# Kernel optimization log

Measured on AMD Instinct MI355X. Metric: run time of the kernel, lower is better.

The kernel has to match this reference:

```python
import jax, jax.numpy as jnp
import numpy as np

N = 50000      # nodes
E = 800000     # edges
D_IN = 128
D_H = 256
D_OUT = 128
EPS = 1e-5
SLOPE = 0.01   # LeakyReLU negative_slope


def setup_inputs() -> dict:
    key = jax.random.key(0)
    ks = jax.random.split(key, 24)
    inp = {}
    inp["x"] = jax.random.normal(ks[0], (N, D_IN), dtype=jnp.float32)
    inp["edge_index"] = jax.random.randint(ks[1], (2, E), 0, N, dtype=jnp.int32)
    dims = [(D_IN, D_H), (D_H, D_H), (D_H, D_H), (D_H, D_OUT)]
    for i, (di, do) in enumerate(dims, start=1):
        inp[f"W{i}"] = jax.random.normal(ks[4 * i - 2], (di, do), dtype=jnp.float32) / np.float32(np.sqrt(di))
        inp[f"b{i}"] = jnp.zeros((do,), dtype=jnp.float32)
        inp[f"g{i}"] = 1.0 + 0.1 * jax.random.normal(ks[4 * i - 1], (do,), dtype=jnp.float32)   # BN gamma
        inp[f"be{i}"] = 0.1 * jax.random.normal(ks[4 * i], (do,), dtype=jnp.float32)            # BN beta
    inp["ln_g"] = 1.0 + 0.1 * jax.random.normal(ks[18], (D_OUT,), dtype=jnp.float32)
    inp["ln_b"] = 0.1 * jax.random.normal(ks[19], (D_OUT,), dtype=jnp.float32)
    return inp


def _gcn_conv(x, W, b, src, dst, nisq):
    # PyG GCNConv: linear first, then sym-normalized aggregation with self-loops.
    xl = x @ W                                   # [N, do]
    coef = (nisq[src] * nisq[dst])[:, None]      # [E, 1]
    msg = xl[src] * coef                         # [E, do] gather
    agg = jax.ops.segment_sum(msg, dst, num_segments=N)  # scatter-add
    # self-loop contribution: deg^{-1/2}_i * deg^{-1/2}_i * xl_i
    return agg + xl * (nisq * nisq)[:, None] + b


def _bn(x, g, b):
    # BatchNorm1d, training-mode batch statistics (biased variance)
    m = jnp.mean(x, axis=0)
    v = jnp.var(x, axis=0)
    return (x - m) * jax.lax.rsqrt(v + EPS) * g + b


def _lrelu(x):
    return jnp.where(x >= 0, x, SLOPE * x)


def _layer_norm(x, g, b):
    m = jnp.mean(x, axis=-1, keepdims=True)
    v = jnp.var(x, axis=-1, keepdims=True)
    return (x - m) * jax.lax.rsqrt(v + EPS) * g + b


def reference(x, edge_index, W1, b1, g1, be1, W2, b2, g2, be2, W3, b3, g3, be3, W4, b4, g4, be4, ln_g, ln_b):
    src = edge_index[0]
    dst = edge_index[1]
    # degrees with self-loops (computed once, shared by all 4 convs)
    deg = jax.ops.segment_sum(jnp.ones((E,), dtype=x.dtype), dst, num_segments=N) + 1.0
    nisq = jax.lax.rsqrt(deg)  # deg >= 1 so safe

    identity = x  # input_dim == output_dim -> residual_fc is Identity
    h = _lrelu(_bn(_gcn_conv(x, W1, b1, src, dst, nisq), g1, be1))   # dropout = identity (eval)
    h = _lrelu(_bn(_gcn_conv(h, W2, b2, src, dst, nisq), g2, be2))
    h = _lrelu(_bn(_gcn_conv(h, W3, b3, src, dst, nisq), g3, be3))
    h = _gcn_conv(h, W4, b4, src, dst, nisq)
    h = h + identity
    return _layer_norm(_bn(h, g4, be4), ln_g, ln_b)
```

## Files before the change

kernel.cpp:

```cpp
#include <hip/hip_runtime.h>

#define N_NODES 50000
#define N_EDGES 800000
#define EPS_C 1e-5f
#define SLOPE_C 0.01f

typedef __attribute__((ext_vector_type(8))) short short8v;
typedef __attribute__((ext_vector_type(4))) float f32x4;

__device__ __forceinline__ unsigned short f2bf(float f) {
  unsigned u = __float_as_uint(f);
  u += 0x7fffu + ((u >> 16) & 1u);
  return (unsigned short)(u >> 16);
}
__device__ __forceinline__ unsigned packbf(float a, float b) {
  return (unsigned)f2bf(a) | ((unsigned)f2bf(b) << 16);
}
__device__ __forceinline__ float bflo(unsigned u) { return __uint_as_float(u << 16); }
__device__ __forceinline__ float bfhi(unsigned u) { return __uint_as_float(u & 0xffff0000u); }

__global__ void wcast_kernel(const float* __restrict__ W, unsigned short* __restrict__ Wt,
                             int total, int mshift, int mmask, int K) {
  const int idx = blockIdx.x * 256 + threadIdx.x;
  if (idx >= total) return;
  const int k = idx >> mshift;
  const int m = idx & mmask;
  Wt[(size_t)m * K + k] = f2bf(W[idx]);
}

template <bool NISQ_EPI, bool BF16OUT>
__global__ __launch_bounds__(256) void gemm_mfma_kernel(
    const unsigned short* __restrict__ A, const unsigned short* __restrict__ Wt,
    const float* __restrict__ aux, void* __restrict__ Yv,
    int Nrows, int K, int M) {
  __shared__ __align__(16) unsigned short As[128][72];
  __shared__ __align__(16) unsigned short Bs[64][72];
  const int tid = threadIdx.x;
  const int lane = tid & 63;
  const int wave = tid >> 6;
  const int wr = wave >> 1, wc = wave & 1;
  const int row0 = blockIdx.x * 128;
  const int col0 = blockIdx.y * 64;
  const int l15 = lane & 15;
  const int lhi = lane >> 4;
  f32x4 acc[4][2];
#pragma unroll
  for (int i = 0; i < 4; ++i)
#pragma unroll
    for (int j = 0; j < 2; ++j) acc[i][j] = (f32x4){0.f, 0.f, 0.f, 0.f};

  for (int k0 = 0; k0 < K; k0 += 64) {
#pragma unroll
    for (int c = 0; c < 4; ++c) {
      const int id = tid + c * 256;
      const int r = id >> 3;
      const int ck = (id & 7) * 8;
      short8v v = {};
      const int grow = row0 + r;
      if (grow < Nrows)
        v = *reinterpret_cast<const short8v*>(&A[(size_t)grow * K + k0 + ck]);
      *reinterpret_cast<short8v*>(&As[r][ck]) = v;
    }
#pragma unroll
    for (int c = 0; c < 2; ++c) {
      const int id = tid + c * 256;
      const int r = id >> 3;
      const int ck = (id & 7) * 8;
      const short8v v =
          *reinterpret_cast<const short8v*>(&Wt[(size_t)(col0 + r) * K + k0 + ck]);
      *reinterpret_cast<short8v*>(&Bs[r][ck]) = v;
    }
    __syncthreads();
    short8v bfr[2][2];
#pragma unroll
    for (int nr = 0; nr < 2; ++nr)
#pragma unroll
      for (int h = 0; h < 2; ++h)
        bfr[nr][h] = *reinterpret_cast<const short8v*>(
            &Bs[wc * 32 + nr * 16 + l15][h * 32 + lhi * 8]);
#pragma unroll
    for (int mr = 0; mr < 4; ++mr) {
#pragma unroll
      for (int h = 0; h < 2; ++h) {
        const short8v af = *reinterpret_cast<const short8v*>(
            &As[wr * 64 + mr * 16 + l15][h * 32 + lhi * 8]);
#pragma unroll
        for (int nr = 0; nr < 2; ++nr)
          acc[mr][nr] = __builtin_amdgcn_mfma_f32_16x16x32_bf16(
              af, bfr[nr][h], acc[mr][nr], 0, 0, 0);
      }
    }
    __syncthreads();
  }
#pragma unroll
  for (int mr = 0; mr < 4; ++mr) {
#pragma unroll
    for (int r = 0; r < 4; ++r) {
      const int grow = row0 + wr * 64 + mr * 16 + lhi * 4 + r;
      if (grow < Nrows) {
        if constexpr (NISQ_EPI) {
          const float s = aux[grow];
          unsigned short* Y = (unsigned short*)Yv;
#pragma unroll
          for (int nr = 0; nr < 2; ++nr) {
            const int gcol = col0 + wc * 32 + nr * 16 + l15;
            Y[(size_t)grow * M + gcol] = f2bf(acc[mr][nr][r] * s);
          }
        } else {
          float* Y = (float*)Yv;
#pragma unroll
          for (int nr = 0; nr < 2; ++nr) {
            const int gcol = col0 + wc * 32 + nr * 16 + l15;
            Y[(size_t)grow * M + gcol] = acc[mr][nr][r] + aux[gcol];
          }
        }
      }
    }
  }
}

__global__ void hist_kernel(const int* __restrict__ dst, int* __restrict__ hist, int E) {
  const int e = blockIdx.x * 256 + threadIdx.x;
  if (e < E) atomicAdd(&hist[dst[e]], 1);
}

__global__ void nisq_kernel(const int* __restrict__ hist, float* __restrict__ nisq, int n) {
  const int i = blockIdx.x * 256 + threadIdx.x;
  if (i < n) nisq[i] = rsqrtf((float)hist[i] + 1.0f);
}

__global__ __launch_bounds__(1024) void scan1_kernel(
    const int* __restrict__ hist, int* __restrict__ off, int* __restrict__ partial, int n) {
  __shared__ int tmp[1024];
  const int tid = threadIdx.x;
  const int i = blockIdx.x * 1024 + tid;
  const int v = (i < n) ? hist[i] : 0;
  tmp[tid] = v;
  __syncthreads();
  int x = v;
  for (int o = 1; o < 1024; o <<= 1) {
    const int y = (tid >= o) ? tmp[tid - o] : 0;
    __syncthreads();
    x += y;
    tmp[tid] = x;
    __syncthreads();
  }
  if (i < n) off[i] = x - v;
  if (tid == 1023) partial[blockIdx.x] = x;
}

__global__ __launch_bounds__(64) void scan2_kernel(
    const int* __restrict__ partial, int* __restrict__ partialoff,
    int* __restrict__ offN, int nb) {
  const int tid = threadIdx.x;
  const int v = (tid < nb) ? partial[tid] : 0;
  int x = v;
  for (int o = 1; o < 64; o <<= 1) {
    const int y = __shfl_up(x, o, 64);
    if (tid >= o) x += y;
  }
  if (tid < nb) partialoff[tid] = x - v;
  if (tid == 63) *offN = x;
}

__global__ void scan3_kernel(int* __restrict__ off, int* __restrict__ cursor,
                             const int* __restrict__ partialoff, int n) {
  const int i = blockIdx.x * 256 + threadIdx.x;
  if (i < n) {
    const int o = off[i] + partialoff[i >> 10];
    off[i] = o;
    cursor[i] = o;
  }
}

__global__ void scatter_kernel(const int* __restrict__ src, const int* __restrict__ dst,
                               int* __restrict__ cursor, int* __restrict__ esorted, int E) {
  const int e = blockIdx.x * 256 + threadIdx.x;
  if (e < E) {
    const int p = atomicAdd(&cursor[dst[e]], 1);
    esorted[p] = src[e];
  }
}

__global__ void scale_cast_kernel(const float* __restrict__ x,
                                  const float* __restrict__ nisq,
                                  unsigned short* __restrict__ xs) {
  const int idx = blockIdx.x * 256 + threadIdx.x;
  if (idx >= N_NODES * 32) return;
  const int row = idx >> 5;
  const int c = (idx & 31) * 4;
  const float s = nisq[row];
  const float4 v = *reinterpret_cast<const float4*>(&x[(size_t)row * 128 + c]);
  ushort4 o;
  o.x = f2bf(v.x * s); o.y = f2bf(v.y * s);
  o.z = f2bf(v.z * s); o.w = f2bf(v.w * s);
  *reinterpret_cast<ushort4*>(&xs[(size_t)row * 128 + c]) = o;
}

template <int DO, bool ADD_BIAS, bool HAS_RES, bool OUT_BF16, bool STATS>
__global__ __launch_bounds__(256) void aggregate2_kernel(
    const unsigned short* __restrict__ Y, const int* __restrict__ segoff,
    const int* __restrict__ esorted, const float* __restrict__ nisq,
    const float* __restrict__ bias, const float* __restrict__ resid,
    void* __restrict__ Tv, float* __restrict__ split) {
  constexpr int V2 = DO / 32;
  const int wave = threadIdx.x >> 6;
  const int lane = threadIdx.x & 63;
  const int half = lane >> 5;
  const int l31 = lane & 31;
  const int n = blockIdx.x * 4 + wave;
  const int colbase = l31 * V2;
  float a0[V2], a1[V2], vals[V2];
#pragma unroll
  for (int i = 0; i < V2; ++i) { a0[i] = 0.f; a1[i] = 0.f; vals[i] = 0.f; }
  const bool valid = (n < N_NODES);
  if (valid) {
    const int s = segoff[n];
    const int e = segoff[n + 1];
    auto addrow = [&](float* a, int rid) {
      const unsigned short* yr = Y + (size_t)rid * DO + colbase;
      if constexpr (V2 == 8) {
        const uint4 v = *reinterpret_cast<const uint4*>(yr);
        a[0] += bflo(v.x); a[1] += bfhi(v.x);
        a[2] += bflo(v.y); a[3] += bfhi(v.y);
        a[4] += bflo(v.z); a[5] += bfhi(v.z);
        a[6] += bflo(v.w); a[7] += bfhi(v.w);
      } else {
        const uint2 v = *reinterpret_cast<const uint2*>(yr);
        a[0] += bflo(v.x); a[1] += bfhi(v.x);
        a[2] += bflo(v.y); a[3] += bfhi(v.y);
      }
    };
    int j = s + half;
    for (; j + 2 < e; j += 4) {
      const int i0 = esorted[j];
      const int i1 = esorted[j + 2];
      addrow(a0, i0);
      addrow(a1, i1);
    }
    if (j < e) addrow(a0, esorted[j]);
    if (half == 0) addrow(a1, n);
    const float sc = nisq[n];
#pragma unroll
    for (int i = 0; i < V2; ++i) {
      float t = a0[i] + a1[i];
      t += __shfl_xor(t, 32, 64);
      t *= sc;
      if (half == 0) {
        if (ADD_BIAS) t += bias[colbase + i];
        if (HAS_RES) t += resid[(size_t)n * DO + colbase + i];
      }
      vals[i] = t;
    }
    if (half == 0) {
      if constexpr (OUT_BF16) {
        unsigned short* tr = (unsigned short*)Tv + (size_t)n * DO + colbase;
        if constexpr (V2 == 8) {
          uint4 o;
          o.x = packbf(vals[0], vals[1]); o.y = packbf(vals[2], vals[3]);
          o.z = packbf(vals[4], vals[5]); o.w = packbf(vals[6], vals[7]);
          *reinterpret_cast<uint4*>(tr) = o;
        } else {
          uint2 o;
          o.x = packbf(vals[0], vals[1]); o.y = packbf(vals[2], vals[3]);
          *reinterpret_cast<uint2*>(tr) = o;
        }
      } else {
        float* tr = (float*)Tv + (size_t)n * DO + colbase;
        if constexpr (V2 == 8) {
          float4 o0 = {vals[0], vals[1], vals[2], vals[3]};
          float4 o1 = {vals[4], vals[5], vals[6], vals[7]};
          *reinterpret_cast<float4*>(tr) = o0;
          *reinterpret_cast<float4*>(tr + 4) = o1;
        } else {
          float4 o = {vals[0], vals[1], vals[2], vals[3]};
          *reinterpret_cast<float4*>(tr) = o;
        }
      }
    }
  }
  if constexpr (STATS) {
    __shared__ float spart[4][DO];
    if (half == 0) {
#pragma unroll
      for (int i = 0; i < V2; ++i) spart[wave][colbase + i] = vals[i];
    }
    __syncthreads();
    const int tid = threadIdx.x;
    if (tid < DO) {
      float s = 0.f, q = 0.f;
#pragma unroll
      for (int w = 0; w < 4; ++w) {
        const float v = spart[w][tid];
        s += v;
        q += v * v;
      }
      const int sb = (blockIdx.x & 63) * 2 * DO;
      atomicAdd(&split[sb + tid], s);
      atomicAdd(&split[sb + DO + tid], q);
    }
  }
}

__global__ void reduce_stats_kernel(const float* __restrict__ split,
                                    float* __restrict__ colsum,
                                    float* __restrict__ colsumsq, int DO) {
  const int c = threadIdx.x;
  if (c >= DO) return;
  float s = 0.f, q = 0.f;
  for (int k = 0; k < 64; ++k) {
    s += split[k * 2 * DO + c];
    q += split[k * 2 * DO + DO + c];
  }
  colsum[c] = s;
  colsumsq[c] = q;
}

__global__ void stats_kernel(const float* __restrict__ T, float* __restrict__ colsum,
                             float* __restrict__ colsumsq, int n, int rowsPerBlock) {
  const int c = threadIdx.x;
  const int DO = blockDim.x;
  const int r0 = blockIdx.x * rowsPerBlock;
  int r1 = r0 + rowsPerBlock;
  if (r1 > n) r1 = n;
  float s = 0.f, q = 0.f;
  for (int r = r0; r < r1; ++r) {
    const float v = T[(size_t)r * DO + c];
    s += v;
    q += v * v;
  }
  atomicAdd(&colsum[c], s);
  atomicAdd(&colsumsq[c], q);
}

__global__ void bn_lrelu_bf16_kernel(const float* __restrict__ T,
                                     const float* __restrict__ colsum,
                                     const float* __restrict__ colsumsq,
                                     const float* __restrict__ g, const float* __restrict__ be,
                                     unsigned short* __restrict__ Tb,
                                     size_t total4, unsigned domask4, float invN) {
  const size_t idx = (size_t)blockIdx.x * 256 + threadIdx.x;
  if (idx >= total4) return;
  const unsigned c = ((unsigned)idx & domask4) * 4;
  const float4 cs = *reinterpret_cast<const float4*>(&colsum[c]);
  const float4 cq = *reinterpret_cast<const float4*>(&colsumsq[c]);
  const float4 gv = *reinterpret_cast<const float4*>(&g[c]);
  const float4 bv = *reinterpret_cast<const float4*>(&be[c]);
  const float4 t = *reinterpret_cast<const float4*>(&T[idx * 4]);
  const float m0 = cs.x * invN, m1 = cs.y * invN, m2 = cs.z * invN, m3 = cs.w * invN;
  const float r0 = rsqrtf(cq.x * invN - m0 * m0 + EPS_C);
  const float r1 = rsqrtf(cq.y * invN - m1 * m1 + EPS_C);
  const float r2 = rsqrtf(cq.z * invN - m2 * m2 + EPS_C);
  const float r3 = rsqrtf(cq.w * invN - m3 * m3 + EPS_C);
  float z0 = (t.x - m0) * r0 * gv.x + bv.x; z0 = (z0 >= 0.f) ? z0 : SLOPE_C * z0;
  float z1 = (t.y - m1) * r1 * gv.y + bv.y; z1 = (z1 >= 0.f) ? z1 : SLOPE_C * z1;
  float z2 = (t.z - m2) * r2 * gv.z + bv.z; z2 = (z2 >= 0.f) ? z2 : SLOPE_C * z2;
  float z3 = (t.w - m3) * r3 * gv.w + bv.w; z3 = (z3 >= 0.f) ? z3 : SLOPE_C * z3;
  ushort4 o;
  o.x = f2bf(z0); o.y = f2bf(z1); o.z = f2bf(z2); o.w = f2bf(z3);
  *reinterpret_cast<ushort4*>(&Tb[idx * 4]) = o;
}

__global__ void bn_lrelu_ip_kernel(unsigned short* __restrict__ Tb,
                                   const float* __restrict__ colsum,
                                   const float* __restrict__ colsumsq,
                                   const float* __restrict__ g, const float* __restrict__ be,
                                   size_t total8, unsigned mask8, float invN) {
  const size_t idx = (size_t)blockIdx.x * 256 + threadIdx.x;
  if (idx >= total8) return;
  const unsigned c = ((unsigned)idx & mask8) * 8;
  uint4 v = *reinterpret_cast<uint4*>(&Tb[idx * 8]);
  float z[8] = {bflo(v.x), bfhi(v.x), bflo(v.y), bfhi(v.y),
                bflo(v.z), bfhi(v.z), bflo(v.w), bfhi(v.w)};
  const float4 cs0 = *reinterpret_cast<const float4*>(&colsum[c]);
  const float4 cs1 = *reinterpret_cast<const float4*>(&colsum[c + 4]);
  const float4 cq0 = *reinterpret_cast<const float4*>(&colsumsq[c]);
  const float4 cq1 = *reinterpret_cast<const float4*>(&colsumsq[c + 4]);
  const float4 gv0 = *reinterpret_cast<const float4*>(&g[c]);
  const float4 gv1 = *reinterpret_cast<const float4*>(&g[c + 4]);
  const float4 bv0 = *reinterpret_cast<const float4*>(&be[c]);
  const float4 bv1 = *reinterpret_cast<const float4*>(&be[c + 4]);
  const float css[8] = {cs0.x, cs0.y, cs0.z, cs0.w, cs1.x, cs1.y, cs1.z, cs1.w};
  const float cqq[8] = {cq0.x, cq0.y, cq0.z, cq0.w, cq1.x, cq1.y, cq1.z, cq1.w};
  const float ggg[8] = {gv0.x, gv0.y, gv0.z, gv0.w, gv1.x, gv1.y, gv1.z, gv1.w};
  const float bbb[8] = {bv0.x, bv0.y, bv0.z, bv0.w, bv1.x, bv1.y, bv1.z, bv1.w};
#pragma unroll
  for (int k = 0; k < 8; ++k) {
    const float m = css[k] * invN;
    const float rs = rsqrtf(cqq[k] * invN - m * m + EPS_C);
    float zz = (z[k] - m) * rs * ggg[k] + bbb[k];
    z[k] = (zz >= 0.f) ? zz : SLOPE_C * zz;
  }
  v.x = packbf(z[0], z[1]); v.y = packbf(z[2], z[3]);
  v.z = packbf(z[4], z[5]); v.w = packbf(z[6], z[7]);
  *reinterpret_cast<uint4*>(&Tb[idx * 8]) = v;
}

__global__ __launch_bounds__(256) void bn_ln_kernel(
    const float* __restrict__ T, const float* __restrict__ colsum,
    const float* __restrict__ colsumsq, const float* __restrict__ g,
    const float* __restrict__ be, const float* __restrict__ lng,
    const float* __restrict__ lnb, float* __restrict__ out, float invN) {
  const int wave = threadIdx.x >> 6;
  const int lane = threadIdx.x & 63;
  const int n = blockIdx.x * 4 + wave;
  if (n >= N_NODES) return;
  const int c = lane * 2;
  const float2 t = *reinterpret_cast<const float2*>(&T[(size_t)n * 128 + c]);
  float z[2];
#pragma unroll
  for (int k = 0; k < 2; ++k) {
    const float m = colsum[c + k] * invN;
    const float v = colsumsq[c + k] * invN - m * m;
    const float tv = (k == 0) ? t.x : t.y;
    z[k] = (tv - m) * rsqrtf(v + EPS_C) * g[c + k] + be[c + k];
  }
  float s = z[0] + z[1];
  float q = z[0] * z[0] + z[1] * z[1];
  for (int o = 32; o > 0; o >>= 1) {
    s += __shfl_xor(s, o, 64);
    q += __shfl_xor(q, o, 64);
  }
  const float mean = s * (1.f / 128.f);
  const float var = q * (1.f / 128.f) - mean * mean;
  const float rs = rsqrtf(var + EPS_C);
  float2 o2;
  o2.x = (z[0] - mean) * rs * lng[c] + lnb[c];
  o2.y = (z[1] - mean) * rs * lng[c + 1] + lnb[c + 1];
  *reinterpret_cast<float2*>(&out[(size_t)n * 128 + c]) = o2;
}

extern "C" void kernel_launch(void* const* d_in, const int* in_sizes, int n_in,
                              void* d_out, int out_size, void* d_ws, size_t ws_size,
                              hipStream_t stream) {
  const float* x = (const float*)d_in[0];
  const int* ei = (const int*)d_in[1];
  const int* srcp = ei;
  const int* dstp = ei + N_EDGES;
  const float* W1 = (const float*)d_in[2];
  const float* b1 = (const float*)d_in[3];
  const float* g1 = (const float*)d_in[4];
  const float* be1 = (const float*)d_in[5];
  const float* W2 = (const float*)d_in[6];
  const float* b2 = (const float*)d_in[7];
  const float* g2 = (const float*)d_in[8];
  const float* be2 = (const float*)d_in[9];
  const float* W3 = (const float*)d_in[10];
  const float* b3 = (const float*)d_in[11];
  const float* g3 = (const float*)d_in[12];
  const float* be3 = (const float*)d_in[13];
  const float* W4 = (const float*)d_in[14];
  const float* b4 = (const float*)d_in[15];
  const float* g4 = (const float*)d_in[16];
  const float* be4 = (const float*)d_in[17];
  const float* lng = (const float*)d_in[18];
  const float* lnb = (const float*)d_in[19];
  float* out = (float*)d_out;

  char* ws = (char*)d_ws;
  size_t off_b = 0;
  auto alloc = [&](size_t bytes) -> void* {
    void* p = (void*)(ws + off_b);
    off_b += (bytes + 255) & ~(size_t)255;
    return p;
  };
  int* hist = (int*)alloc((size_t)N_NODES * 4);
  int* segoff = (int*)alloc((size_t)(N_NODES + 1) * 4);
  int* cursor = (int*)alloc((size_t)N_NODES * 4);
  float* nisq = (float*)alloc((size_t)N_NODES * 4);
  int* esorted = (int*)alloc((size_t)N_EDGES * 4);
  int* partial = (int*)alloc(64 * 4);
  int* partialoff = (int*)alloc(64 * 4);
  float* colsum = (float*)alloc(256 * 4);
  float* colsumsq = (float*)alloc(256 * 4);
  float* split = (float*)alloc((size_t)64 * 2 * 256 * 4);
  unsigned short* Wt1 = (unsigned short*)alloc((size_t)256 * 128 * 2);
  unsigned short* Wt2 = (unsigned short*)alloc((size_t)256 * 256 * 2);
  unsigned short* Wt3 = (unsigned short*)alloc((size_t)256 * 256 * 2);
  unsigned short* Wt4 = (unsigned short*)alloc((size_t)128 * 256 * 2);
  float* T = (float*)alloc((size_t)N_NODES * 256 * 4);
  unsigned short* B1 = (unsigned short*)alloc((size_t)N_NODES * 256 * 2);
  unsigned short* B2 = (unsigned short*)alloc((size_t)N_NODES * 256 * 2);
  unsigned short* Ybf = (unsigned short*)alloc((size_t)N_NODES * 256 * 2);
  unsigned short* xsb = Ybf;
  unsigned short* xaB = Ybf + (size_t)N_NODES * 128;

  const float invN = 1.0f / (float)N_NODES;
  const int egrid = (N_EDGES + 255) / 256;
  const int ngrid = (N_NODES + 255) / 256;
  const int aggrid = (N_NODES + 3) / 4;
  const int statgrid = (N_NODES + 127) / 128;
  const int nb = (N_NODES + 1023) / 1024;
  const dim3 mgrid256((N_NODES + 127) / 128, 4);
  const dim3 mgrid128((N_NODES + 127) / 128, 2);
  const unsigned bngrid_f32 = (unsigned)(((size_t)N_NODES * 64 + 255) / 256);
  const unsigned bngrid_ip = (unsigned)(((size_t)N_NODES * 32 + 255) / 256);

  hipMemsetAsync(hist, 0, (size_t)N_NODES * 4, stream);
  hist_kernel<<<egrid, 256, 0, stream>>>(dstp, hist, N_EDGES);
  nisq_kernel<<<ngrid, 256, 0, stream>>>(hist, nisq, N_NODES);
  scan1_kernel<<<nb, 1024, 0, stream>>>(hist, segoff, partial, N_NODES);
  scan2_kernel<<<1, 64, 0, stream>>>(partial, partialoff, &segoff[N_NODES], nb);
  scan3_kernel<<<ngrid, 256, 0, stream>>>(segoff, cursor, partialoff, N_NODES);
  scatter_kernel<<<egrid, 256, 0, stream>>>(srcp, dstp, cursor, esorted, N_EDGES);

  wcast_kernel<<<(128 * 256 + 255) / 256, 256, 0, stream>>>(W1, Wt1, 128 * 256, 8, 255, 128);
  wcast_kernel<<<(256 * 256 + 255) / 256, 256, 0, stream>>>(W2, Wt2, 256 * 256, 8, 255, 256);
  wcast_kernel<<<(256 * 256 + 255) / 256, 256, 0, stream>>>(W3, Wt3, 256 * 256, 8, 255, 256);
  wcast_kernel<<<(256 * 128 + 255) / 256, 256, 0, stream>>>(W4, Wt4, 256 * 128, 7, 127, 256);

  scale_cast_kernel<<<(N_NODES * 32 + 255) / 256, 256, 0, stream>>>(x, nisq, xsb);
  aggregate2_kernel<128, false, false, true, false><<<aggrid, 256, 0, stream>>>(
      xsb, segoff, esorted, nisq, nullptr, nullptr, xaB, nullptr);
  gemm_mfma_kernel<false, false><<<mgrid256, 256, 0, stream>>>(xaB, Wt1, b1, T, N_NODES, 128, 256);
  hipMemsetAsync(colsum, 0, 2048, stream);
  stats_kernel<<<statgrid, 256, 0, stream>>>(T, colsum, colsumsq, N_NODES, 128);
  bn_lrelu_bf16_kernel<<<bngrid_f32, 256, 0, stream>>>(T, colsum, colsumsq, g1, be1, B1,
                                                       (size_t)N_NODES * 64, 63u, invN);

  gemm_mfma_kernel<true, true><<<mgrid256, 256, 0, stream>>>(B1, Wt2, nisq, Ybf, N_NODES, 256, 256);
  hipMemsetAsync(split, 0, (size_t)64 * 2 * 256 * 4, stream);
  aggregate2_kernel<256, true, false, true, true><<<aggrid, 256, 0, stream>>>(
      Ybf, segoff, esorted, nisq, b2, nullptr, B2, split);
  reduce_stats_kernel<<<1, 256, 0, stream>>>(split, colsum, colsumsq, 256);
  bn_lrelu_ip_kernel<<<bngrid_ip, 256, 0, stream>>>(B2, colsum, colsumsq, g2, be2,
                                                    (size_t)N_NODES * 32, 31u, invN);

  gemm_mfma_kernel<true, true><<<mgrid256, 256, 0, stream>>>(B2, Wt3, nisq, Ybf, N_NODES, 256, 256);
  hipMemsetAsync(split, 0, (size_t)64 * 2 * 256 * 4, stream);
  aggregate2_kernel<256, true, false, true, true><<<aggrid, 256, 0, stream>>>(
      Ybf, segoff, esorted, nisq, b3, nullptr, B1, split);
  reduce_stats_kernel<<<1, 256, 0, stream>>>(split, colsum, colsumsq, 256);
  bn_lrelu_ip_kernel<<<bngrid_ip, 256, 0, stream>>>(B1, colsum, colsumsq, g3, be3,
                                                    (size_t)N_NODES * 32, 31u, invN);

  gemm_mfma_kernel<true, true><<<mgrid128, 256, 0, stream>>>(B1, Wt4, nisq, Ybf, N_NODES, 256, 128);
  hipMemsetAsync(split, 0, (size_t)64 * 2 * 128 * 4, stream);
  aggregate2_kernel<128, true, true, false, true><<<aggrid, 256, 0, stream>>>(
      Ybf, segoff, esorted, nisq, b4, x, T, split);
  reduce_stats_kernel<<<1, 128, 0, stream>>>(split, colsum, colsumsq, 128);
  bn_ln_kernel<<<aggrid, 256, 0, stream>>>(T, colsum, colsumsq, g4, be4, lng, lnb, out, invN);
}
```

Before: 589.6 us.

## Aggregate before GEMM in middle layers and fuse BN stats into GEMM epilogue

Layers 2 and 3 now aggregate the BN/LeakyReLU output first and then run the GEMM, matching layer 1. The GEMM epilogue adds the bias, writes bf16 and accumulates per-column sum and sum-of-squares through shared memory and global atomics. The separate stats split buffer, the reduce kernels and the f32 intermediate for layer 1 are removed, and the nisq pre-scale moves into the BN/LeakyReLU kernel, which writes a new table. This cuts kernel launches and memory traffic, at the cost of BN statistics taken from unrounded values while normalising bf16-rounded values, plus contended column atomics. Layer 4 keeps GEMM-first and now runs the stats kernel with 128 threads instead of 256.

```diff
diff --git a/kernel.cpp b/kernel.cpp
--- a/kernel.cpp
+++ b/kernel.cpp
@@ -28,13 +28,15 @@
   Wt[(size_t)m * K + k] = f2bf(W[idx]);
 }
 
-template <bool NISQ_EPI, bool BF16OUT>
+template <int MODE>
 __global__ __launch_bounds__(256) void gemm_mfma_kernel(
     const unsigned short* __restrict__ A, const unsigned short* __restrict__ Wt,
-    const float* __restrict__ aux, void* __restrict__ Yv,
+    const float* __restrict__ bias, unsigned short* __restrict__ Yb,
+    float* __restrict__ colsum, float* __restrict__ colsumsq,
     int Nrows, int K, int M) {
   __shared__ __align__(16) unsigned short As[128][72];
   __shared__ __align__(16) unsigned short Bs[64][72];
+  __shared__ float sred[2][64][8];
   const int tid = threadIdx.x;
   const int lane = tid & 63;
   const int wave = tid >> 6;
@@ -92,29 +94,49 @@
     }
     __syncthreads();
   }
+  float bcol[2] = {0.f, 0.f};
+  if constexpr (MODE == 1) {
+#pragma unroll
+    for (int nr = 0; nr < 2; ++nr) bcol[nr] = bias[col0 + wc * 32 + nr * 16 + l15];
+  }
+  float s_c[2] = {0.f, 0.f}, q_c[2] = {0.f, 0.f};
 #pragma unroll
   for (int mr = 0; mr < 4; ++mr) {
 #pragma unroll
     for (int r = 0; r < 4; ++r) {
       const int grow = row0 + wr * 64 + mr * 16 + lhi * 4 + r;
-      if (grow < Nrows) {
-        if constexpr (NISQ_EPI) {
-          const float s = aux[grow];
-          unsigned short* Y = (unsigned short*)Yv;
-#pragma unroll
-          for (int nr = 0; nr < 2; ++nr) {
-            const int gcol = col0 + wc * 32 + nr * 16 + l15;
-            Y[(size_t)grow * M + gcol] = f2bf(acc[mr][nr][r] * s);
-          }
-        } else {
-          float* Y = (float*)Yv;
-#pragma unroll
-          for (int nr = 0; nr < 2; ++nr) {
-            const int gcol = col0 + wc * 32 + nr * 16 + l15;
-            Y[(size_t)grow * M + gcol] = acc[mr][nr][r] + aux[gcol];
+      const bool ok = (grow < Nrows);
+#pragma unroll
+      for (int nr = 0; nr < 2; ++nr) {
+        const int gcol = col0 + wc * 32 + nr * 16 + l15;
+        float v = acc[mr][nr][r] + bcol[nr];
+        if (ok) {
+          Yb[(size_t)grow * M + gcol] = f2bf(v);
+          if constexpr (MODE == 1) {
+            s_c[nr] += v;
+            q_c[nr] += v * v;
           }
         }
       }
+    }
+  }
+  if constexpr (MODE == 1) {
+    const int contrib = wr * 4 + lhi;
+#pragma unroll
+    for (int nr = 0; nr < 2; ++nr) {
+      const int cl = wc * 32 + nr * 16 + l15;
+      sred[0][cl][contrib] = s_c[nr];
+      sred[1][cl][contrib] = q_c[nr];
+    }
+    __syncthreads();
+    if (tid < 128) {
+      const int which = tid >> 6;
+      const int cl = tid & 63;
+      float acc8 = 0.f;
+#pragma unroll
+      for (int k = 0; k < 8; ++k) acc8 += sred[which][cl][k];
+      float* dstp = which ? colsumsq : colsum;
+      atomicAdd(&dstp[col0 + cl], acc8);
     }
   }
 }
@@ -197,123 +219,87 @@
   *reinterpret_cast<ushort4*>(&xs[(size_t)row * 128 + c]) = o;
 }
 
-template <int DO, bool ADD_BIAS, bool HAS_RES, bool OUT_BF16, bool STATS>
-__global__ __launch_bounds__(256) void aggregate2_kernel(
+template <int DO, bool ADD_BIAS, bool HAS_RES, bool OUT_BF16>
+__global__ __launch_bounds__(256) void aggregate3_kernel(
     const unsigned short* __restrict__ Y, const int* __restrict__ segoff,
     const int* __restrict__ esorted, const float* __restrict__ nisq,
     const float* __restrict__ bias, const float* __restrict__ resid,
-    void* __restrict__ Tv, float* __restrict__ split) {
+    void* __restrict__ Tv) {
   constexpr int V2 = DO / 32;
   const int wave = threadIdx.x >> 6;
   const int lane = threadIdx.x & 63;
   const int half = lane >> 5;
   const int l31 = lane & 31;
   const int n = blockIdx.x * 4 + wave;
+  if (n >= N_NODES) return;
   const int colbase = l31 * V2;
-  float a0[V2], a1[V2], vals[V2];
-#pragma unroll
-  for (int i = 0; i < V2; ++i) { a0[i] = 0.f; a1[i] = 0.f; vals[i] = 0.f; }
-  const bool valid = (n < N_NODES);
-  if (valid) {
-    const int s = segoff[n];
-    const int e = segoff[n + 1];
-    auto addrow = [&](float* a, int rid) {
-      const unsigned short* yr = Y + (size_t)rid * DO + colbase;
+  float a0[V2], a1[V2];
+#pragma unroll
+  for (int i = 0; i < V2; ++i) { a0[i] = 0.f; a1[i] = 0.f; }
+  const int s = segoff[n];
+  const int e = segoff[n + 1];
+  auto addrow = [&](float* a, int rid) {
+    const unsigned short* yr = Y + (size_t)rid * DO + colbase;
+    if constexpr (V2 == 8) {
+      const uint4 v = *reinterpret_cast<const uint4*>(yr);
+      a[0] += bflo(v.x); a[1] += bfhi(v.x);
+      a[2] += bflo(v.y); a[3] += bfhi(v.y);
+      a[4] += bflo(v.z); a[5] += bfhi(v.z);
+      a[6] += bflo(v.w); a[7] += bfhi(v.w);
+    } else {
+      const uint2 v = *reinterpret_cast<const uint2*>(yr);
+      a[0] += bflo(v.x); a[1] += bfhi(v.x);
+      a[2] += bflo(v.y); a[3] += bfhi(v.y);
+    }
+  };
+  int j = s + half;
+  for (; j + 2 < e; j += 4) {
+    const int i0 = esorted[j];
+    const int i1 = esorted[j + 2];
+    addrow(a0, i0);
+    addrow(a1, i1);
+  }
+  if (j < e) addrow(a0, esorted[j]);
+  if (half == 0) addrow(a1, n);
+  const float sc = nisq[n];
+  float vals[V2];
+#pragma unroll
+  for (int i = 0; i < V2; ++i) {
+    float t = a0[i] + a1[i];
+    t += __shfl_xor(t, 32, 64);
+    t *= sc;
+    if (half == 0) {
+      if (ADD_BIAS) t += bias[colbase + i];
+      if (HAS_RES) t += resid[(size_t)n * DO + colbase + i];
+    }
+    vals[i] = t;
+  }
+  if (half == 0) {
+    if constexpr (OUT_BF16) {
+      unsigned short* tr = (unsigned short*)Tv + (size_t)n * DO + colbase;
       if constexpr (V2 == 8) {
-        const uint4 v = *reinterpret_cast<const uint4*>(yr);
-        a[0] += bflo(v.x); a[1] += bfhi(v.x);
-        a[2] += bflo(v.y); a[3] += bfhi(v.y);
-        a[4] += bflo(v.z); a[5] += bfhi(v.z);
-        a[6] += bflo(v.w); a[7] += bfhi(v.w);
+        uint4 o;
+        o.x = packbf(vals[0], vals[1]); o.y = packbf(vals[2], vals[3]);
+        o.z = packbf(vals[4], vals[5]); o.w = packbf(vals[6], vals[7]);
+        *reinterpret_cast<uint4*>(tr) = o;
       } else {
-        const uint2 v = *reinterpret_cast<const uint2*>(yr);
-        a[0] += bflo(v.x); a[1] += bfhi(v.x);
-        a[2] += bflo(v.y); a[3] += bfhi(v.y);
+        uint2 o;
+        o.x = packbf(vals[0], vals[1]); o.y = packbf(vals[2], vals[3]);
+        *reinterpret_cast<uint2*>(tr) = o;
       }
-    };
-    int j = s + half;
-    for (; j + 2 < e; j += 4) {
-      const int i0 = esorted[j];
-      const int i1 = esorted[j + 2];
-      addrow(a0, i0);
-      addrow(a1, i1);
-    }
-    if (j < e) addrow(a0, esorted[j]);
-    if (half == 0) addrow(a1, n);
-    const float sc = nisq[n];
-#pragma unroll
-    for (int i = 0; i < V2; ++i) {
-      float t = a0[i] + a1[i];
-      t += __shfl_xor(t, 32, 64);
-      t *= sc;
-      if (half == 0) {
-        if (ADD_BIAS) t += bias[colbase + i];
-        if (HAS_RES) t += resid[(size_t)n * DO + colbase + i];
+    } else {
+      float* tr = (float*)Tv + (size_t)n * DO + colbase;
+      if constexpr (V2 == 8) {
+        float4 o0 = {vals[0], vals[1], vals[2], vals[3]};
+        float4 o1 = {vals[4], vals[5], vals[6], vals[7]};
+        *reinterpret_cast<float4*>(tr) = o0;
+        *reinterpret_cast<float4*>(tr + 4) = o1;
+      } else {
+        float4 o = {vals[0], vals[1], vals[2], vals[3]};
+        *reinterpret_cast<float4*>(tr) = o;
       }
-      vals[i] = t;
-    }
-    if (half == 0) {
-      if constexpr (OUT_BF16) {
-        unsigned short* tr = (unsigned short*)Tv + (size_t)n * DO + colbase;
-        if constexpr (V2 == 8) {
-          uint4 o;
-          o.x = packbf(vals[0], vals[1]); o.y = packbf(vals[2], vals[3]);
-          o.z = packbf(vals[4], vals[5]); o.w = packbf(vals[6], vals[7]);
-          *reinterpret_cast<uint4*>(tr) = o;
-        } else {
-          uint2 o;
-          o.x = packbf(vals[0], vals[1]); o.y = packbf(vals[2], vals[3]);
-          *reinterpret_cast<uint2*>(tr) = o;
-        }
-      } else {
-        float* tr = (float*)Tv + (size_t)n * DO + colbase;
-        if constexpr (V2 == 8) {
-          float4 o0 = {vals[0], vals[1], vals[2], vals[3]};
-          float4 o1 = {vals[4], vals[5], vals[6], vals[7]};
-          *reinterpret_cast<float4*>(tr) = o0;
-          *reinterpret_cast<float4*>(tr + 4) = o1;
-        } else {
-          float4 o = {vals[0], vals[1], vals[2], vals[3]};
-          *reinterpret_cast<float4*>(tr) = o;
-        }
-      }
-    }
-  }
-  if constexpr (STATS) {
-    __shared__ float spart[4][DO];
-    if (half == 0) {
-#pragma unroll
-      for (int i = 0; i < V2; ++i) spart[wave][colbase + i] = vals[i];
-    }
-    __syncthreads();
-    const int tid = threadIdx.x;
-    if (tid < DO) {
-      float s = 0.f, q = 0.f;
-#pragma unroll
-      for (int w = 0; w < 4; ++w) {
-        const float v = spart[w][tid];
-        s += v;
-        q += v * v;
-      }
-      const int sb = (blockIdx.x & 63) * 2 * DO;
-      atomicAdd(&split[sb + tid], s);
-      atomicAdd(&split[sb + DO + tid], q);
-    }
-  }
-}
-
-__global__ void reduce_stats_kernel(const float* __restrict__ split,
-                                    float* __restrict__ colsum,
-                                    float* __restrict__ colsumsq, int DO) {
-  const int c = threadIdx.x;
-  if (c >= DO) return;
-  float s = 0.f, q = 0.f;
-  for (int k = 0; k < 64; ++k) {
-    s += split[k * 2 * DO + c];
-    q += split[k * 2 * DO + DO + c];
-  }
-  colsum[c] = s;
-  colsumsq[c] = q;
+    }
+  }
 }
 
 __global__ void stats_kernel(const float* __restrict__ T, float* __restrict__ colsum,
@@ -333,43 +319,19 @@
   atomicAdd(&colsumsq[c], q);
 }
 
-__global__ void bn_lrelu_bf16_kernel(const float* __restrict__ T,
+__global__ void bn_lrelu_nisq_kernel(const unsigned short* __restrict__ Tb,
                                      const float* __restrict__ colsum,
                                      const float* __restrict__ colsumsq,
                                      const float* __restrict__ g, const float* __restrict__ be,
-                                     unsigned short* __restrict__ Tb,
-                                     size_t total4, unsigned domask4, float invN) {
-  const size_t idx = (size_t)blockIdx.x * 256 + threadIdx.x;
-  if (idx >= total4) return;
-  const unsigned c = ((unsigned)idx & domask4) * 4;
-  const float4 cs = *reinterpret_cast<const float4*>(&colsum[c]);
-  const float4 cq = *reinterpret_cast<const float4*>(&colsumsq[c]);
-  const float4 gv = *reinterpret_cast<const float4*>(&g[c]);
-  const float4 bv = *reinterpret_cast<const float4*>(&be[c]);
-  const float4 t = *reinterpret_cast<const float4*>(&T[idx * 4]);
-  const float m0 = cs.x * invN, m1 = cs.y * invN, m2 = cs.z * invN, m3 = cs.w * invN;
-  const float r0 = rsqrtf(cq.x * invN - m0 * m0 + EPS_C);
-  const float r1 = rsqrtf(cq.y * invN - m1 * m1 + EPS_C);
-  const float r2 = rsqrtf(cq.z * invN - m2 * m2 + EPS_C);
-  const float r3 = rsqrtf(cq.w * invN - m3 * m3 + EPS_C);
-  float z0 = (t.x - m0) * r0 * gv.x + bv.x; z0 = (z0 >= 0.f) ? z0 : SLOPE_C * z0;
-  float z1 = (t.y - m1) * r1 * gv.y + bv.y; z1 = (z1 >= 0.f) ? z1 : SLOPE_C * z1;
-  float z2 = (t.z - m2) * r2 * gv.z + bv.z; z2 = (z2 >= 0.f) ? z2 : SLOPE_C * z2;
-  float z3 = (t.w - m3) * r3 * gv.w + bv.w; z3 = (z3 >= 0.f) ? z3 : SLOPE_C * z3;
-  ushort4 o;
-  o.x = f2bf(z0); o.y = f2bf(z1); o.z = f2bf(z2); o.w = f2bf(z3);
-  *reinterpret_cast<ushort4*>(&Tb[idx * 4]) = o;
-}
-
-__global__ void bn_lrelu_ip_kernel(unsigned short* __restrict__ Tb,
-                                   const float* __restrict__ colsum,
-                                   const float* __restrict__ colsumsq,
-                                   const float* __restrict__ g, const float* __restrict__ be,
-                                   size_t total8, unsigned mask8, float invN) {
+                                     const float* __restrict__ nisq,
+                                     unsigned short* __restrict__ outb,
+                                     size_t total8, float invN) {
   const size_t idx = (size_t)blockIdx.x * 256 + threadIdx.x;
   if (idx >= total8) return;
-  const unsigned c = ((unsigned)idx & mask8) * 8;
-  uint4 v = *reinterpret_cast<uint4*>(&Tb[idx * 8]);
+  const unsigned c = ((unsigned)idx & 31u) * 8;
+  const int row = (int)(idx >> 5);
+  const float sc = nisq[row];
+  uint4 v = *reinterpret_cast<const uint4*>(&Tb[idx * 8]);
   float z[8] = {bflo(v.x), bfhi(v.x), bflo(v.y), bfhi(v.y),
                 bflo(v.z), bfhi(v.z), bflo(v.w), bfhi(v.w)};
   const float4 cs0 = *reinterpret_cast<const float4*>(&colsum[c]);
@@ -389,11 +351,12 @@
     const float m = css[k] * invN;
     const float rs = rsqrtf(cqq[k] * invN - m * m + EPS_C);
     float zz = (z[k] - m) * rs * ggg[k] + bbb[k];
-    z[k] = (zz >= 0.f) ? zz : SLOPE_C * zz;
+    zz = (zz >= 0.f) ? zz : SLOPE_C * zz;
+    z[k] = zz * sc;
   }
   v.x = packbf(z[0], z[1]); v.y = packbf(z[2], z[3]);
   v.z = packbf(z[4], z[5]); v.w = packbf(z[6], z[7]);
-  *reinterpret_cast<uint4*>(&Tb[idx * 8]) = v;
+  *reinterpret_cast<uint4*>(&outb[idx * 8]) = v;
 }
 
 __global__ __launch_bounds__(256) void bn_ln_kernel(
@@ -473,17 +436,15 @@
   int* partialoff = (int*)alloc(64 * 4);
   float* colsum = (float*)alloc(256 * 4);
   float* colsumsq = (float*)alloc(256 * 4);
-  float* split = (float*)alloc((size_t)64 * 2 * 256 * 4);
   unsigned short* Wt1 = (unsigned short*)alloc((size_t)256 * 128 * 2);
   unsigned short* Wt2 = (unsigned short*)alloc((size_t)256 * 256 * 2);
   unsigned short* Wt3 = (unsigned short*)alloc((size_t)256 * 256 * 2);
   unsigned short* Wt4 = (unsigned short*)alloc((size_t)128 * 256 * 2);
-  float* T = (float*)alloc((size_t)N_NODES * 256 * 4);
-  unsigned short* B1 = (unsigned short*)alloc((size_t)N_NODES * 256 * 2);
-  unsigned short* B2 = (unsigned short*)alloc((size_t)N_NODES * 256 * 2);
-  unsigned short* Ybf = (unsigned short*)alloc((size_t)N_NODES * 256 * 2);
-  unsigned short* xsb = Ybf;
-  unsigned short* xaB = Ybf + (size_t)N_NODES * 128;
+  unsigned short* tblA = (unsigned short*)alloc((size_t)N_NODES * 256 * 2);
+  unsigned short* tblB = (unsigned short*)alloc((size_t)N_NODES * 256 * 2);
+  unsigned short* S = (unsigned short*)alloc((size_t)N_NODES * 256 * 2);
+  unsigned short* Tb = (unsigned short*)alloc((size_t)N_NODES * 256 * 2);
+  float* Tf = (float*)alloc((size_t)N_NODES * 128 * 4);
 
   const float invN = 1.0f / (float)N_NODES;
   const int egrid = (N_EDGES + 255) / 256;
@@ -493,8 +454,7 @@
   const int nb = (N_NODES + 1023) / 1024;
   const dim3 mgrid256((N_NODES + 127) / 128, 4);
   const dim3 mgrid128((N_NODES + 127) / 128, 2);
-  const unsigned bngrid_f32 = (unsigned)(((size_t)N_NODES * 64 + 255) / 256);
-  const unsigned bngrid_ip = (unsigned)(((size_t)N_NODES * 32 + 255) / 256);
+  const unsigned bngrid = (unsigned)(((size_t)N_NODES * 32 + 255) / 256);
 
   hipMemsetAsync(hist, 0, (size_t)N_NODES * 4, stream);
   hist_kernel<<<egrid, 256, 0, stream>>>(dstp, hist, N_EDGES);
@@ -509,35 +469,36 @@
   wcast_kernel<<<(256 * 256 + 255) / 256, 256, 0, stream>>>(W3, Wt3, 256 * 256, 8, 255, 256);
   wcast_kernel<<<(256 * 128 + 255) / 256, 256, 0, stream>>>(W4, Wt4, 256 * 128, 7, 127, 256);
 
-  scale_cast_kernel<<<(N_NODES * 32 + 255) / 256, 256, 0, stream>>>(x, nisq, xsb);
-  aggregate2_kernel<128, false, false, true, false><<<aggrid, 256, 0, stream>>>(
-      xsb, segoff, esorted, nisq, nullptr, nullptr, xaB, nullptr);
-  gemm_mfma_kernel<false, false><<<mgrid256, 256, 0, stream>>>(xaB, Wt1, b1, T, N_NODES, 128, 256);
+  scale_cast_kernel<<<(N_NODES * 32 + 255) / 256, 256, 0, stream>>>(x, nisq, tblA);
+  aggregate3_kernel<128, false, false, true><<<aggrid, 256, 0, stream>>>(
+      tblA, segoff, esorted, nisq, nullptr, nullptr, S);
   hipMemsetAsync(colsum, 0, 2048, stream);
-  stats_kernel<<<statgrid, 256, 0, stream>>>(T, colsum, colsumsq, N_NODES, 128);
-  bn_lrelu_bf16_kernel<<<bngrid_f32, 256, 0, stream>>>(T, colsum, colsumsq, g1, be1, B1,
-                                                       (size_t)N_NODES * 64, 63u, invN);
-
-  gemm_mfma_kernel<true, true><<<mgrid256, 256, 0, stream>>>(B1, Wt2, nisq, Ybf, N_NODES, 256, 256);
-  hipMemsetAsync(split, 0, (size_t)64 * 2 * 256 * 4, stream);
-  aggregate2_kernel<256, true, false, true, true><<<aggrid, 256, 0, stream>>>(
-      Ybf, segoff, esorted, nisq, b2, nullptr, B2, split);
-  reduce_stats_kernel<<<1, 256, 0, stream>>>(split, colsum, colsumsq, 256);
-  bn_lrelu_ip_kernel<<<bngrid_ip, 256, 0, stream>>>(B2, colsum, colsumsq, g2, be2,
-                                                    (size_t)N_NODES * 32, 31u, invN);
-
-  gemm_mfma_kernel<true, true><<<mgrid256, 256, 0, stream>>>(B2, Wt3, nisq, Ybf, N_NODES, 256, 256);
-  hipMemsetAsync(split, 0, (size_t)64 * 2 * 256 * 4, stream);
-  aggregate2_kernel<256, true, false, true, true><<<aggrid, 256, 0, stream>>>(
-      Ybf, segoff, esorted, nisq, b3, nullptr, B1, split);
-  reduce_stats_kernel<<<1, 256, 0, stream>>>(split, colsum, colsumsq, 256);
-  bn_lrelu_ip_kernel<<<bngrid_ip, 256, 0, stream>>>(B1, colsum, colsumsq, g3, be3,
-                                                    (size_t)N_NODES * 32, 31u, invN);
-
-  gemm_mfma_kernel<true, true><<<mgrid128, 256, 0, stream>>>(B1, Wt4, nisq, Ybf, N_NODES, 256, 128);
-  hipMemsetAsync(split, 0, (size_t)64 * 2 * 128 * 4, stream);
-  aggregate2_kernel<128, true, true, false, true><<<aggrid, 256, 0, stream>>>(
-      Ybf, segoff, esorted, nisq, b4, x, T, split);
-  reduce_stats_kernel<<<1, 128, 0, stream>>>(split, colsum, colsumsq, 128);
-  bn_ln_kernel<<<aggrid, 256, 0, stream>>>(T, colsum, colsumsq, g4, be4, lng, lnb, out, invN);
-}
+  gemm_mfma_kernel<1><<<mgrid256, 256, 0, stream>>>(S, Wt1, b1, Tb, colsum, colsumsq,
+                                                    N_NODES, 128, 256);
+  bn_lrelu_nisq_kernel<<<bngrid, 256, 0, stream>>>(Tb, colsum, colsumsq, g1, be1, nisq,
+                                                   tblB, (size_t)N_NODES * 32, invN);
+
+  aggregate3_kernel<256, false, false, true><<<aggrid, 256, 0, stream>>>(
+      tblB, segoff, esorted, nisq, nullptr, nullptr, S);
+  hipMemsetAsync(colsum, 0, 2048, stream);
+  gemm_mfma_kernel<1><<<mgrid256, 256, 0, stream>>>(S, Wt2, b2, Tb, colsum, colsumsq,
+                                                    N_NODES, 256, 256);
+  bn_lrelu_nisq_kernel<<<bngrid, 256, 0, stream>>>(Tb, colsum, colsumsq, g2, be2, nisq,
+                                                   tblA, (size_t)N_NODES * 32, invN);
+
+  aggregate3_kernel<256, false, false, true><<<aggrid, 256, 0, stream>>>(
+      tblA, segoff, esorted, nisq, nullptr, nullptr, S);
+  hipMemsetAsync(colsum, 0, 2048, stream);
+  gemm_mfma_kernel<1><<<mgrid256, 256, 0, stream>>>(S, Wt3, b3, Tb, colsum, colsumsq,
+                                                    N_NODES, 256, 256);
+  bn_lrelu_nisq_kernel<<<bngrid, 256, 0, stream>>>(Tb, colsum, colsumsq, g3, be3, nisq,
+                                                   tblB, (size_t)N_NODES * 32, invN);
+
+  gemm_mfma_kernel<0><<<mgrid128, 256, 0, stream>>>(tblB, Wt4, nullptr, S, nullptr, nullptr,
+                                                    N_NODES, 256, 128);
+  aggregate3_kernel<128, true, true, false><<<aggrid, 256, 0, stream>>>(
+      S, segoff, esorted, nisq, b4, x, Tf);
+  hipMemsetAsync(colsum, 0, 2048, stream);
+  stats_kernel<<<statgrid, 128, 0, stream>>>(Tf, colsum, colsumsq, N_NODES, 128);
+  bn_ln_kernel<<<aggrid, 256, 0, stream>>>(Tf, colsum, colsumsq, g4, be4, lng, lnb, out, invN);
+}
```

Result: faster. 555.8 us (-5.7%).
